# Kernel tuning notes

Measured on AMD Instinct MI355X. Metric: run time of the kernel, lower is better.

## Reference

```python
import jax, jax.numpy as jnp
import numpy as np

NUM_HEADS = 16
HEAD_DIM = 64
HIDDEN = NUM_HEADS * HEAD_DIM  # 1024
B, T = 32, 512


def setup_inputs() -> dict:
    key = jax.random.key(0)
    ks = jax.random.split(key, 10)
    s = 1.0 / np.sqrt(HIDDEN)
    inp = {
        "x": jax.random.normal(ks[0], (B, HIDDEN, T), dtype=jnp.float32),
        "mask": jax.random.randint(ks[1], (B, T), 0, 2, dtype=jnp.int32),
        "Wq": jax.random.uniform(ks[2], (HIDDEN, HIDDEN), jnp.float32, -s, s),
        "bq": jax.random.uniform(ks[3], (HIDDEN,), jnp.float32, -s, s),
        "Wk": jax.random.uniform(ks[4], (HIDDEN, HIDDEN), jnp.float32, -s, s),
        "bk": jax.random.uniform(ks[5], (HIDDEN,), jnp.float32, -s, s),
        "Wv": jax.random.uniform(ks[6], (HIDDEN, HIDDEN), jnp.float32, -s, s),
        "bv": jax.random.uniform(ks[7], (HIDDEN,), jnp.float32, -s, s),
        "Wo": jax.random.uniform(ks[8], (HIDDEN, HIDDEN), jnp.float32, -s, s),
        "bo": jax.random.uniform(ks[9], (HIDDEN,), jnp.float32, -s, s),
    }
    return inp


def reference(x, mask, Wq, bq, Wk, bk, Wv, bv, Wo, bo):
    # x: [B, hidden, T] -> tokens along last axis
    b, h, t = x.shape
    xt = jnp.swapaxes(x, 1, 2)  # [B, T, hidden]

    def heads(w, bias):
        y = xt @ w.T + bias                       # [B, T, hidden]
        return y.reshape(b, t, NUM_HEADS, HEAD_DIM).transpose(0, 2, 1, 3)  # [B, nh, T, hd]

    q = heads(Wq, bq)
    k = heads(Wk, bk)
    v = heads(Wv, bv)

    scores = jnp.einsum("bhqd,bhkd->bhqk", q, k) / jnp.sqrt(jnp.float32(HEAD_DIM))
    # masked_fill(mask==0, -inf) then clamp to [-50, 50]: masked entries become -50
    scores = jnp.where(mask[:, None, None, :] == 0, -jnp.inf, scores)
    scores = jnp.clip(scores, -50.0, 50.0)
    attn = jax.nn.softmax(scores, axis=-1)        # [B, nh, T, T]
    out = jnp.einsum("bhqk,bhkd->bhqd", attn, v)  # [B, nh, T, hd]
    out = out.transpose(0, 2, 1, 3).reshape(b, t, h)
    out = out @ Wo.T + bo                         # [B, T, hidden]
    return out.max(axis=1)                        # [B, hidden]
```

## Files before the change

kernel.cpp:

```cpp
#include <hip/hip_runtime.h>


typedef _Float16 half8 __attribute__((ext_vector_type(8)));
typedef _Float16 half4 __attribute__((ext_vector_type(4)));
typedef float floatx4 __attribute__((ext_vector_type(4)));
typedef unsigned uintx2 __attribute__((ext_vector_type(2)));

#define HID 1024
#define TT 512
#define NB 32
#define QSCALE 0.1803368801111244f
#define SB2 72.13475204444817f

__device__ __forceinline__ void gload16(const void* g, void* l) {
    __builtin_amdgcn_global_load_lds(
        (const __attribute__((address_space(1))) unsigned int*)g,
        (__attribute__((address_space(3))) unsigned int*)l, 16, 0, 0);
}

__device__ __forceinline__ unsigned fkey(float f) {
    unsigned u = __float_as_uint(f);
    return (u & 0x80000000u) ? ~u : (u | 0x80000000u);
}
__device__ __forceinline__ float funkey(unsigned k) {
    unsigned u = (k & 0x80000000u) ? (k ^ 0x80000000u) : ~k;
    return __uint_as_float(u);
}

__global__ __launch_bounds__(256) void prep_kernel(
    const float* __restrict__ Wq, const float* __restrict__ Wk,
    const float* __restrict__ Wv, const float* __restrict__ Wo,
    _Float16* __restrict__ Wcat,
    const float* __restrict__ x, _Float16* __restrict__ xT,
    unsigned* __restrict__ omax,
    const float* __restrict__ bq, float* __restrict__ bqs,
    const int* __restrict__ mask, short* __restrict__ cp16,
    int* __restrict__ Tcg, _Float16* __restrict__ KT,
    _Float16* __restrict__ Vb)
{
    __shared__ float tile[64][65];
    const int bid = blockIdx.x;
    if (bid < 4096) {
        int i4 = bid * 256 + threadIdx.x;
        int sec = i4 >> 18;
        int off4 = i4 & ((1 << 18) - 1);
        const float* src = (sec == 0) ? Wq : (sec == 1) ? Wk
                          : (sec == 2) ? Wv : Wo;
        float4 v = ((const float4*)src)[off4];
        if (sec == 0) {
            v.x *= QSCALE; v.y *= QSCALE; v.z *= QSCALE; v.w *= QSCALE;
        }
        half4 h = {(_Float16)v.x, (_Float16)v.y, (_Float16)v.z, (_Float16)v.w};
        *(half4*)(Wcat + (size_t)i4 * 4) = h;
    } else if (bid < 8192) {
        int idx = bid - 4096;
        int b = idx >> 7, h0 = ((idx >> 3) & 15) * 64, t0 = (idx & 7) * 64;
        int tx = threadIdx.x & 15, ty = threadIdx.x >> 4;
        const float* xb = x + ((size_t)b * HID + h0) * TT + t0;
        for (int p = 0; p < 4; p++) {
            int r = ty + 16 * p;
            float4 v = *(const float4*)(xb + (size_t)r * TT + tx * 4);
            tile[r][tx * 4 + 0] = v.x;
            tile[r][tx * 4 + 1] = v.y;
            tile[r][tx * 4 + 2] = v.z;
            tile[r][tx * 4 + 3] = v.w;
        }
        __syncthreads();
        int hc = (threadIdx.x & 7) * 8, tb = threadIdx.x >> 3;
        for (int rd = 0; rd < 2; rd++) {
            int tt = tb + 32 * rd;
            half8 pk;
            for (int k = 0; k < 8; k++)
                pk[k] = (_Float16)tile[hc + k][tt];
            *(half8*)(xT + ((size_t)b * TT + t0 + tt) * HID + h0 + hc) = pk;
        }
    } else if (bid < 8320) {
        omax[(bid - 8192) * 256 + threadIdx.x] = 0u;
    } else if (bid < 8324) {
        int i = (bid - 8320) * 256 + threadIdx.x;
        bqs[i] = bq[i] * QSCALE;
    } else {
        __shared__ int wsum[4];
        __shared__ int tcs;
        const int b = bid - 8324;
        const int* mrow = mask + b * TT;
        const int tid = threadIdx.x;
        const int lane = tid & 63, wv = tid >> 6;
        const int m0 = mrow[tid * 2] ? 1 : 0;
        const int m1 = mrow[tid * 2 + 1] ? 1 : 0;
        const int ps = m0 + m1;
        int v = ps;
        for (int d = 1; d < 64; d <<= 1) {
            int u = __shfl_up(v, d, 64);
            if (lane >= d) v += u;
        }
        if (lane == 63) wsum[wv] = v;
        __syncthreads();
        int off = 0;
        for (int i = 0; i < 4; i++) off += (i < wv) ? wsum[i] : 0;
        const int excl = off + v - ps;
        cp16[(size_t)b * TT + tid * 2]     = m0 ? (short)excl : (short)-1;
        cp16[(size_t)b * TT + tid * 2 + 1] = m1 ? (short)(excl + m0) : (short)-1;
        if (tid == 255) { tcs = off + v; Tcg[b] = off + v; }
        __syncthreads();
        const int Tcv = tcs;
        const int ce = (Tcv + 63) & ~63;
        const int nrow = ce - Tcv;
        half8 z8 = {};
        _Float16* kb = KT + ((size_t)b * TT + Tcv) * HID;
        for (int i = tid; i < nrow * 128; i += 256) ((half8*)kb)[i] = z8;
        for (int o = tid; o < 1024; o += 256) {
            _Float16* vr = Vb + ((size_t)b * HID + o) * TT;
            for (int j = 0; j < nrow; j++) vr[Tcv + j] = (_Float16)0.f;
        }
    }
}

#define PH_PRE do { \
    __builtin_amdgcn_s_barrier(); \
    asm volatile("s_waitcnt lgkmcnt(0)" ::: "memory"); \
    __builtin_amdgcn_sched_barrier(0); \
    __builtin_amdgcn_s_setprio(1); \
} while (0)

#define PH_POST(N) do { \
    __builtin_amdgcn_s_setprio(0); \
    asm volatile("s_waitcnt vmcnt(" #N ")" ::: "memory"); \
    __builtin_amdgcn_s_barrier(); \
} while (0)

#define LDA(P, MH) do { \
    const _Float16* ab_ = lds + (P) * 16384 + (MH) * 8192 + aoff; \
    af[0][0] = *(const half8*)(ab_ + pb0); \
    af[0][1] = *(const half8*)(ab_ + pb1); \
    af[1][0] = *(const half8*)(ab_ + 1024 + pb0); \
    af[1][1] = *(const half8*)(ab_ + 1024 + pb1); \
    af[2][0] = *(const half8*)(ab_ + 2048 + pb0); \
    af[2][1] = *(const half8*)(ab_ + 2048 + pb1); \
    af[3][0] = *(const half8*)(ab_ + 3072 + pb0); \
    af[3][1] = *(const half8*)(ab_ + 3072 + pb1); \
} while (0)

#define LDB(P, NH) do { \
    const _Float16* bb_ = lds + 32768 + (P) * 16384 + (NH) * 8192 + boff; \
    bf[NH][0][0] = *(const half8*)(bb_ + pb0); \
    bf[NH][0][1] = *(const half8*)(bb_ + pb1); \
    bf[NH][1][0] = *(const half8*)(bb_ + 1024 + pb0); \
    bf[NH][1][1] = *(const half8*)(bb_ + 1024 + pb1); \
} while (0)

#define MFMAQ(MH, NH) do { \
    _Pragma("unroll") \
    for (int j_ = 0; j_ < 4; ++j_) { \
        _Pragma("unroll") \
        for (int n_ = 0; n_ < 2; ++n_) { \
            floatx4 c_ = acc[(MH) * 4 + j_][(NH) * 2 + n_]; \
            c_ = __builtin_amdgcn_mfma_f32_16x16x32_f16( \
                af[j_][0], bf[NH][n_][0], c_, 0, 0, 0); \
            c_ = __builtin_amdgcn_mfma_f32_16x16x32_f16( \
                af[j_][1], bf[NH][n_][1], c_, 0, 0, 0); \
            acc[(MH) * 4 + j_][(NH) * 2 + n_] = c_; \
        } \
    } \
} while (0)

#define STAGE_A(P, MH, K0) do { \
    _Float16* d_ = lds + (P) * 16384 + (MH) * 8192 + wst; \
    gload16(ag + (MH) * 65536 + (K0), d_); \
    gload16(ag + 131072 + (MH) * 65536 + (K0), d_ + 4096); \
} while (0)

#define STAGE_B(P, NH, K0) do { \
    _Float16* d_ = lds + 32768 + (P) * 16384 + (NH) * 8192 + wst; \
    gload16(bg + (NH) * 32768 + (K0), d_); \
    gload16(bg + 131072 + (NH) * 32768 + (K0), d_ + 4096); \
} while (0)

__device__ __forceinline__ void mainloop256(
    const _Float16* __restrict__ Ag,
    const _Float16* __restrict__ Bg,
    _Float16* lds, floatx4 acc[8][4], int tid)
{
    const int lane = tid & 63;
    const int w = tid >> 6, wr = w >> 2, wc = w & 3;
    const int l15 = lane & 15, quad = lane >> 4;
    const int pa = quad ^ (l15 & 7);
    const int pb0 = pa * 8, pb1 = (pa ^ 4) * 8;
    const int aoff = (wr * 64 + l15) * 64;
    const int boff = (wc * 32 + l15) * 64;
    const int wst = w * 512;
    const int r = tid >> 3;
    const int sg = (tid & 7) ^ (r & 7);
    const int nbase = ((r >> 5) << 6) + (r & 31);
    const _Float16* ag = Ag + (size_t)r * 1024 + sg * 8;
    const _Float16* bg = Bg + (size_t)nbase * 1024 + sg * 8;

    half8 af[4][2], bf[2][2][2];

    STAGE_A(0, 0, 0); STAGE_B(0, 0, 0); STAGE_B(0, 1, 0); STAGE_A(0, 1, 0);
    STAGE_A(1, 0, 64); STAGE_B(1, 0, 64); STAGE_B(1, 1, 64);
    asm volatile("s_waitcnt vmcnt(10)" ::: "memory");
    __builtin_amdgcn_s_barrier();

    for (int i = 0; i < 7; ++i) {
        const int kb = i * 128 + 64;
        const int kn0 = kb + 64, kn1 = kb + 128;
        LDA(0, 0); LDB(0, 0); STAGE_A(1, 1, kb);
        PH_PRE; MFMAQ(0, 0); PH_POST(10);
        LDB(0, 1);            STAGE_A(0, 0, kn0);
        PH_PRE; MFMAQ(0, 1); PH_POST(10);
        LDA(0, 1);            STAGE_B(0, 0, kn0);
        PH_PRE; MFMAQ(1, 1); PH_POST(10);
                              STAGE_B(0, 1, kn0);
        PH_PRE; MFMAQ(1, 0); PH_POST(10);
        LDA(1, 0); LDB(1, 0); STAGE_A(0, 1, kn0);
        PH_PRE; MFMAQ(0, 0); PH_POST(10);
        LDB(1, 1);            STAGE_A(1, 0, kn1);
        PH_PRE; MFMAQ(0, 1); PH_POST(10);
        LDA(1, 1);            STAGE_B(1, 0, kn1);
        PH_PRE; MFMAQ(1, 1); PH_POST(10);
                              STAGE_B(1, 1, kn1);
        PH_PRE; MFMAQ(1, 0); PH_POST(10);
    }
    LDA(0, 0); LDB(0, 0); STAGE_A(1, 1, 960);
    PH_PRE; MFMAQ(0, 0); PH_POST(10);
    LDB(0, 1);
    PH_PRE; MFMAQ(0, 1); PH_POST(8);
    LDA(0, 1);
    PH_PRE; MFMAQ(1, 1); PH_POST(6);
    PH_PRE; MFMAQ(1, 0); PH_POST(4);
    LDA(1, 0); LDB(1, 0);
    PH_PRE; MFMAQ(0, 0); PH_POST(2);
    LDB(1, 1);
    PH_PRE; MFMAQ(0, 1); PH_POST(0);
    LDA(1, 1);
    PH_PRE; MFMAQ(1, 1); MFMAQ(1, 0);
    __builtin_amdgcn_s_setprio(0);
}

__global__ __launch_bounds__(512, 2) void gemm1_kernel(
    const _Float16* __restrict__ Wcat,
    const float* __restrict__ bqs, const float* __restrict__ bk,
    const float* __restrict__ bv,
    const _Float16* __restrict__ xT,
    _Float16* __restrict__ QT, _Float16* __restrict__ KT,
    _Float16* __restrict__ Vb, const short* __restrict__ cp16)
{
    __shared__ __align__(16) _Float16 smem[65536];
    const int tid = threadIdx.x;
    const int id = blockIdx.x;
    const int xcd = id & 7, slot = id >> 3;
    const int grp = xcd + 8 * (slot / 12);
    const int m0 = (slot % 12) * 256;
    const int n0 = (grp & 1) * 256;
    const int bb = grp >> 1;
    const int lane = tid & 63;
    const int w = tid >> 6, wr = w >> 2, wc = w & 3;
    const int l15 = lane & 15, quad = lane >> 4;

    floatx4 acc[8][4] = {};
    mainloop256(Wcat + (size_t)m0 * 1024,
                xT + ((size_t)bb * TT + n0) * HID, smem, acc, tid);
    __syncthreads();

    const int sec = m0 >> 10;
    const int mo = m0 & 1023;

    if (sec < 2) {
        const float* bias = (sec == 0) ? bqs : bk;
        _Float16* dst = (sec == 0) ? QT : KT;
        _Float16* tr = smem;
        for (int h = 0; h < 2; ++h) {
            if (wr == h) {
                for (int mi = 0; mi < 8; ++mi) {
                    float bs[4];
                    for (int rr = 0; rr < 4; ++rr)
                        bs[rr] = bias[mo + h * 128 + mi * 16 + quad * 4 + rr];
                    for (int ni = 0; ni < 4; ++ni) {
                        half4 pk;
                        for (int rr = 0; rr < 4; ++rr)
                            pk[rr] = (_Float16)(acc[mi][ni][rr] + bs[rr]);
                        *(half4*)(tr + (wc * 64 + ni * 16 + l15) * 136 +
                                  mi * 16 + quad * 4) = pk;
                    }
                }
            }
            __syncthreads();
            const int row = tid >> 4, off = (tid & 15) * 8;
            for (int s = 0; s < 8; ++s) {
                uint4 v = *(uint4*)(tr + (row + 32 * s) * 136 + off);
                if (sec == 0) {
                    *(uint4*)(dst + ((size_t)bb * TT + n0 + row + 32 * s) * HID +
                              mo + h * 128 + off) = v;
                } else {
                    short cp = cp16[bb * TT + n0 + row + 32 * s];
                    if (cp >= 0)
                        *(uint4*)(dst + ((size_t)bb * TT + cp) * HID +
                                  mo + h * 128 + off) = v;
                }
            }
            __syncthreads();
        }
    } else {
        short cps[4];
        for (int ni = 0; ni < 4; ++ni)
            cps[ni] = cp16[bb * TT + n0 + wc * 64 + ni * 16 + l15];
        for (int mi = 0; mi < 8; ++mi) {
            float bs[4];
            for (int rr = 0; rr < 4; ++rr)
                bs[rr] = bv[mo + wr * 128 + mi * 16 + quad * 4 + rr];
            for (int ni = 0; ni < 4; ++ni) {
                if (cps[ni] < 0) continue;
                for (int rr = 0; rr < 4; ++rr) {
                    int o = mo + wr * 128 + mi * 16 + quad * 4 + rr;
                    Vb[((size_t)bb * HID + o) * TT + cps[ni]] =
                        (_Float16)(acc[mi][ni][rr] + bs[rr]);
                }
            }
        }
    }
}

__global__ __launch_bounds__(512, 4) void attn_kernel(
    const _Float16* __restrict__ QT, const _Float16* __restrict__ KT,
    const _Float16* __restrict__ Vb, const int* __restrict__ Tcg,
    _Float16* __restrict__ OcT)
{
    __shared__ __align__(16) _Float16 kvbuf[4 * 4096];
    __shared__ __align__(16) _Float16 ps[2 * 8192];
    __shared__ __align__(16) float msf[2][64];

    const int id = blockIdx.x;
    const int xcd = id & 7, slot = id >> 3;
    const int grp = xcd + 8 * (slot >> 1);
    const int q0 = (slot & 1) * 256;
    const int hd = grp & 15, b = grp >> 4;
    const int tid = threadIdx.x;
    const int lane = tid & 63, wid = tid >> 6;
    const int l15 = lane & 15, quad = lane >> 4;

    const _Float16* QTb = QT + ((size_t)b * TT + q0) * HID + hd * 64;
    const _Float16* KTb = KT + (size_t)b * TT * HID + hd * 64;
    const _Float16* Vbb = Vb + ((size_t)b * HID + hd * 64) * TT;
    const int Tc = Tcg[b];
    const int nt = (Tc + 63) >> 6;

    const int srow = lane >> 3;
    const int sg = (lane & 7) ^ srow;
    const int pa = quad ^ (l15 & 7);
    const int pz = l15 & 7;

    for (int p = 0; p < 4; p++) {
        int r = p * 64 + wid * 8 + srow;
        gload16(QTb + (size_t)r * HID + sg * 8,
                kvbuf + (p * 64 + wid * 8) * 64);
    }
    __syncthreads();
    half8 bq[2][2];
    for (int qt = 0; qt < 2; qt++) {
        int qr = qt * 128 + wid * 16 + l15;
        bq[qt][0] = *(half8*)(kvbuf + qr * 64 + pa * 8);
        bq[qt][1] = *(half8*)(kvbuf + qr * 64 + (pa ^ 4) * 8);
    }
    __syncthreads();

    auto stage = [&](int jcn, int bufn) {
        int t0n = jcn * 64;
        _Float16* kd = kvbuf + bufn * 4096;
        _Float16* vd = kvbuf + (2 + bufn) * 4096;
        int r = wid * 8 + srow;
        gload16(KTb + (size_t)(t0n + r) * HID + sg * 8, kd + (wid * 8) * 64);
        gload16(Vbb + (size_t)r * TT + t0n + sg * 8, vd + (wid * 8) * 64);
        if (tid < 64) msf[bufn][tid] = (t0n + tid < Tc) ? SB2 : -SB2;
    };

    stage(0, 0);

    floatx4 oacc[2][4] = {};
    float rs[2] = {0.f, 0.f};
    const float lo = -SB2;

    for (int jc = 0; jc < nt; jc++) {
        const int cur = jc & 1;
        __syncthreads();
        if (jc < nt - 1) stage(jc + 1, 1 - cur);

        const _Float16* ks = kvbuf + cur * 4096;
        const _Float16* vs = kvbuf + (2 + cur) * 4096;

        for (int jt = 0; jt < 4; jt++) {
            half8 ka0 = *(half8*)(ks + (jt * 16 + l15) * 64 + pa * 8);
            half8 ka1 = *(half8*)(ks + (jt * 16 + l15) * 64 + (pa ^ 4) * 8);
            floatx4 hi = *(floatx4*)(&msf[cur][jt * 16 + quad * 4]);
            for (int qt = 0; qt < 2; qt++) {
                floatx4 sc = {0.f, 0.f, 0.f, 0.f};
                sc = __builtin_amdgcn_mfma_f32_16x16x32_f16(ka0, bq[qt][0], sc, 0, 0, 0);
                sc = __builtin_amdgcn_mfma_f32_16x16x32_f16(ka1, bq[qt][1], sc, 0, 0, 0);
                float e0 = __builtin_amdgcn_exp2f(fminf(fmaxf(sc[0], lo), hi[0]));
                float e1 = __builtin_amdgcn_exp2f(fminf(fmaxf(sc[1], lo), hi[1]));
                float e2 = __builtin_amdgcn_exp2f(fminf(fmaxf(sc[2], lo), hi[2]));
                float e3 = __builtin_amdgcn_exp2f(fminf(fmaxf(sc[3], lo), hi[3]));
                rs[qt] += (e0 + e1) + (e2 + e3);
                unsigned uA = __builtin_bit_cast(
                    unsigned, __builtin_amdgcn_cvt_pkrtz(e0, e1));
                unsigned uB = __builtin_bit_cast(
                    unsigned, __builtin_amdgcn_cvt_pkrtz(e2, e3));
                uintx2 uv = {uA, uB};
                half4 pk = __builtin_bit_cast(half4, uv);
                int g = jt * 2 + (quad >> 1);
                *(half4*)(ps + qt * 8192 + (wid * 16 + l15) * 64 + (g ^ pz) * 8 +
                          (quad & 1) * 4) = pk;
            }
        }
        for (int kc = 0; kc < 2; kc++) {
            int g = kc * 4 + quad;
            half8 bv8[4];
            for (int d4 = 0; d4 < 4; d4++)
                bv8[d4] = *(half8*)(vs + (d4 * 16 + l15) * 64 + (g ^ pz) * 8);
            for (int qt = 0; qt < 2; qt++) {
                half8 ap = *(half8*)(ps + qt * 8192 + (wid * 16 + l15) * 64 +
                                     (g ^ pz) * 8);
                for (int d4 = 0; d4 < 4; d4++)
                    oacc[qt][d4] = __builtin_amdgcn_mfma_f32_16x16x32_f16(
                        ap, bv8[d4], oacc[qt][d4], 0, 0, 0);
            }
        }
    }

    for (int qt = 0; qt < 2; qt++) {
        float s = rs[qt];
        s += __shfl_xor(s, 16, 64);
        s += __shfl_xor(s, 32, 64);
        s = 1.0f / s;
        float inv[4];
        for (int r = 0; r < 4; r++) inv[r] = __shfl(s, quad * 4 + r, 64);
        for (int d4 = 0; d4 < 4; d4++)
            for (int r = 0; r < 4; r++) {
                int t = q0 + qt * 128 + wid * 16 + quad * 4 + r;
                int c = hd * 64 + d4 * 16 + l15;
                OcT[((size_t)b * TT + t) * HID + c] =
                    (_Float16)(oacc[qt][d4][r] * inv[r]);
            }
    }
}

__global__ __launch_bounds__(512, 2) void gemm2_kernel(
    const _Float16* __restrict__ Wo16, const _Float16* __restrict__ OcT,
    unsigned* __restrict__ omax)
{
    __shared__ __align__(16) _Float16 smem[65536];
    _Float16* lds = smem;
    const int tid = threadIdx.x;
    const int id = blockIdx.x;
    const int xcd = id & 7, slot = id >> 3;
    const int grp = xcd + 8 * (slot >> 2);
    const int m0 = (slot & 3) * 256;
    const int n0 = (grp & 1) * 256;
    const int bb = grp >> 1;
    const int lane = tid & 63;
    const int w = tid >> 6, wr = w >> 2;
    const int l15 = lane & 15, quad = lane >> 4;

    floatx4 acc[8][4] = {};
    mainloop256(Wo16 + (size_t)m0 * 1024,
                OcT + ((size_t)bb * TT + n0) * HID, lds, acc, tid);

    for (int mi = 0; mi < 8; ++mi)
        for (int rr = 0; rr < 4; ++rr) {
            float v = acc[mi][0][rr];
            v = fmaxf(v, acc[mi][1][rr]);
            v = fmaxf(v, acc[mi][2][rr]);
            v = fmaxf(v, acc[mi][3][rr]);
            for (int d = 1; d < 16; d <<= 1)
                v = fmaxf(v, __shfl_xor(v, d, 64));
            if (l15 == 0) {
                int o = m0 + wr * 128 + mi * 16 + quad * 4 + rr;
                atomicMax(&omax[bb * HID + o], fkey(v));
            }
        }
}

__global__ __launch_bounds__(256) void final_kernel(
    const unsigned* __restrict__ omax, const float* __restrict__ bo,
    float* __restrict__ out)
{
    int i = blockIdx.x * 256 + threadIdx.x;
    out[i] = funkey(omax[i]) + bo[i & 1023];
}

extern "C" void kernel_launch(void* const* d_in, const int* in_sizes, int n_in,
                              void* d_out, int out_size, void* d_ws, size_t ws_size,
                              hipStream_t stream)
{
    const float* x  = (const float*)d_in[0];
    const int* mask = (const int*)d_in[1];
    const float* Wq = (const float*)d_in[2];
    const float* bq = (const float*)d_in[3];
    const float* Wk = (const float*)d_in[4];
    const float* bk = (const float*)d_in[5];
    const float* Wv = (const float*)d_in[6];
    const float* bv = (const float*)d_in[7];
    const float* Wo = (const float*)d_in[8];
    const float* bo = (const float*)d_in[9];
    float* out = (float*)d_out;

    char* ws = (char*)d_ws;
    _Float16* Wcat = (_Float16*)(ws);
    _Float16* xT   = (_Float16*)(ws + (8ull  << 20));
    _Float16* QT   = (_Float16*)(ws + (40ull << 20));
    _Float16* KT   = (_Float16*)(ws + (72ull << 20));
    _Float16* Vb   = (_Float16*)(ws + (104ull << 20));
    _Float16* OcT  = (_Float16*)(ws + (136ull << 20));
    unsigned* omax = (unsigned*)(ws + (168ull << 20));
    float*    bqs  = (float*)(ws + (168ull << 20) + (128ull << 10));
    short*    cp16 = (short*)(ws + (168ull << 20) + (132ull << 10));
    int*      Tcg  = (int*)  (ws + (168ull << 20) + (164ull << 10));

    prep_kernel<<<8356, 256, 0, stream>>>(Wq, Wk, Wv, Wo, Wcat, x, xT, omax,
                                          bq, bqs, mask, cp16, Tcg, KT, Vb);
    gemm1_kernel<<<768, 512, 0, stream>>>(Wcat, bqs, bk, bv, xT, QT, KT, Vb,
                                          cp16);
    attn_kernel<<<1024, 512, 0, stream>>>(QT, KT, Vb, Tcg, OcT);
    gemm2_kernel<<<256, 512, 0, stream>>>(Wcat + (3ull << 20), OcT, omax);
    final_kernel<<<128, 256, 0, stream>>>(omax, bo, out);
}
```

Baseline: 320.2 us.

## Compact unmasked tokens before K/V projection and skip empty GEMM tiles

The mask prefix scan moves into its own small kernel that runs first, so the prep kernel can scatter the unmasked tokens of x into a compacted buffer (reusing the OcT workspace). The K and V projection tiles then read this compacted input and return early for column blocks past the padded valid-token count, which avoids the matrix work on masked keys. This adds an extra kernel launch and a serial dependency ahead of prep, plus extra scattered writes of xTc.

```diff
diff --git a/kernel.cpp b/kernel.cpp
--- a/kernel.cpp
+++ b/kernel.cpp
@@ -27,16 +27,55 @@
     return __uint_as_float(u);
 }
 
+__global__ __launch_bounds__(256) void scan_kernel(
+    const int* __restrict__ mask, short* __restrict__ cp16,
+    int* __restrict__ Tcg, _Float16* __restrict__ KT,
+    _Float16* __restrict__ Vb)
+{
+    __shared__ int wsum[4];
+    __shared__ int tcs;
+    const int b = blockIdx.x;
+    const int* mrow = mask + b * TT;
+    const int tid = threadIdx.x;
+    const int lane = tid & 63, wv = tid >> 6;
+    const int m0 = mrow[tid * 2] ? 1 : 0;
+    const int m1 = mrow[tid * 2 + 1] ? 1 : 0;
+    const int ps = m0 + m1;
+    int v = ps;
+    for (int d = 1; d < 64; d <<= 1) {
+        int u = __shfl_up(v, d, 64);
+        if (lane >= d) v += u;
+    }
+    if (lane == 63) wsum[wv] = v;
+    __syncthreads();
+    int off = 0;
+    for (int i = 0; i < 4; i++) off += (i < wv) ? wsum[i] : 0;
+    const int excl = off + v - ps;
+    cp16[(size_t)b * TT + tid * 2]     = m0 ? (short)excl : (short)-1;
+    cp16[(size_t)b * TT + tid * 2 + 1] = m1 ? (short)(excl + m0) : (short)-1;
+    if (tid == 255) { tcs = off + v; Tcg[b] = off + v; }
+    __syncthreads();
+    const int Tcv = tcs;
+    const int ce = (Tcv + 63) & ~63;
+    const int nrow = ce - Tcv;
+    half8 z8 = {};
+    _Float16* kb = KT + ((size_t)b * TT + Tcv) * HID;
+    for (int i = tid; i < nrow * 128; i += 256) ((half8*)kb)[i] = z8;
+    for (int o = tid; o < 1024; o += 256) {
+        _Float16* vr = Vb + ((size_t)b * HID + o) * TT;
+        for (int j = 0; j < nrow; j++) vr[Tcv + j] = (_Float16)0.f;
+    }
+}
+
 __global__ __launch_bounds__(256) void prep_kernel(
     const float* __restrict__ Wq, const float* __restrict__ Wk,
     const float* __restrict__ Wv, const float* __restrict__ Wo,
     _Float16* __restrict__ Wcat,
     const float* __restrict__ x, _Float16* __restrict__ xT,
+    _Float16* __restrict__ xTc,
     unsigned* __restrict__ omax,
     const float* __restrict__ bq, float* __restrict__ bqs,
-    const int* __restrict__ mask, short* __restrict__ cp16,
-    int* __restrict__ Tcg, _Float16* __restrict__ KT,
-    _Float16* __restrict__ Vb)
+    const short* __restrict__ cp16)
 {
     __shared__ float tile[64][65];
     const int bid = blockIdx.x;
@@ -73,46 +112,15 @@
             for (int k = 0; k < 8; k++)
                 pk[k] = (_Float16)tile[hc + k][tt];
             *(half8*)(xT + ((size_t)b * TT + t0 + tt) * HID + h0 + hc) = pk;
+            short ct = cp16[b * TT + t0 + tt];
+            if (ct >= 0)
+                *(half8*)(xTc + ((size_t)b * TT + ct) * HID + h0 + hc) = pk;
         }
     } else if (bid < 8320) {
         omax[(bid - 8192) * 256 + threadIdx.x] = 0u;
-    } else if (bid < 8324) {
+    } else {
         int i = (bid - 8320) * 256 + threadIdx.x;
         bqs[i] = bq[i] * QSCALE;
-    } else {
-        __shared__ int wsum[4];
-        __shared__ int tcs;
-        const int b = bid - 8324;
-        const int* mrow = mask + b * TT;
-        const int tid = threadIdx.x;
-        const int lane = tid & 63, wv = tid >> 6;
-        const int m0 = mrow[tid * 2] ? 1 : 0;
-        const int m1 = mrow[tid * 2 + 1] ? 1 : 0;
-        const int ps = m0 + m1;
-        int v = ps;
-        for (int d = 1; d < 64; d <<= 1) {
-            int u = __shfl_up(v, d, 64);
-            if (lane >= d) v += u;
-        }
-        if (lane == 63) wsum[wv] = v;
-        __syncthreads();
-        int off = 0;
-        for (int i = 0; i < 4; i++) off += (i < wv) ? wsum[i] : 0;
-        const int excl = off + v - ps;
-        cp16[(size_t)b * TT + tid * 2]     = m0 ? (short)excl : (short)-1;
-        cp16[(size_t)b * TT + tid * 2 + 1] = m1 ? (short)(excl + m0) : (short)-1;
-        if (tid == 255) { tcs = off + v; Tcg[b] = off + v; }
-        __syncthreads();
-        const int Tcv = tcs;
-        const int ce = (Tcv + 63) & ~63;
-        const int nrow = ce - Tcv;
-        half8 z8 = {};
-        _Float16* kb = KT + ((size_t)b * TT + Tcv) * HID;
-        for (int i = tid; i < nrow * 128; i += 256) ((half8*)kb)[i] = z8;
-        for (int o = tid; o < 1024; o += 256) {
-            _Float16* vr = Vb + ((size_t)b * HID + o) * TT;
-            for (int j = 0; j < nrow; j++) vr[Tcv + j] = (_Float16)0.f;
-        }
     }
 }
 
@@ -242,9 +250,9 @@
     const _Float16* __restrict__ Wcat,
     const float* __restrict__ bqs, const float* __restrict__ bk,
     const float* __restrict__ bv,
-    const _Float16* __restrict__ xT,
+    const _Float16* __restrict__ xT, const _Float16* __restrict__ xTc,
     _Float16* __restrict__ QT, _Float16* __restrict__ KT,
-    _Float16* __restrict__ Vb, const short* __restrict__ cp16)
+    _Float16* __restrict__ Vb, const int* __restrict__ Tcg)
 {
     __shared__ __align__(16) _Float16 smem[65536];
     const int tid = threadIdx.x;
@@ -258,12 +266,16 @@
     const int w = tid >> 6, wr = w >> 2, wc = w & 3;
     const int l15 = lane & 15, quad = lane >> 4;
 
+    const int sec = m0 >> 10;
+    const int Tc = Tcg[bb];
+    if (sec > 0 && n0 >= ((Tc + 255) & ~255)) return;
+
     floatx4 acc[8][4] = {};
     mainloop256(Wcat + (size_t)m0 * 1024,
-                xT + ((size_t)bb * TT + n0) * HID, smem, acc, tid);
+                ((sec == 0) ? xT : xTc) + ((size_t)bb * TT + n0) * HID,
+                smem, acc, tid);
     __syncthreads();
 
-    const int sec = m0 >> 10;
     const int mo = m0 & 1023;
 
     if (sec < 2) {
@@ -288,32 +300,25 @@
             __syncthreads();
             const int row = tid >> 4, off = (tid & 15) * 8;
             for (int s = 0; s < 8; ++s) {
+                int trow = n0 + row + 32 * s;
                 uint4 v = *(uint4*)(tr + (row + 32 * s) * 136 + off);
-                if (sec == 0) {
-                    *(uint4*)(dst + ((size_t)bb * TT + n0 + row + 32 * s) * HID +
+                if (sec == 0 || trow < Tc)
+                    *(uint4*)(dst + ((size_t)bb * TT + trow) * HID +
                               mo + h * 128 + off) = v;
-                } else {
-                    short cp = cp16[bb * TT + n0 + row + 32 * s];
-                    if (cp >= 0)
-                        *(uint4*)(dst + ((size_t)bb * TT + cp) * HID +
-                                  mo + h * 128 + off) = v;
-                }
             }
             __syncthreads();
         }
     } else {
-        short cps[4];
-        for (int ni = 0; ni < 4; ++ni)
-            cps[ni] = cp16[bb * TT + n0 + wc * 64 + ni * 16 + l15];
         for (int mi = 0; mi < 8; ++mi) {
             float bs[4];
             for (int rr = 0; rr < 4; ++rr)
                 bs[rr] = bv[mo + wr * 128 + mi * 16 + quad * 4 + rr];
             for (int ni = 0; ni < 4; ++ni) {
-                if (cps[ni] < 0) continue;
+                int t = n0 + wc * 64 + ni * 16 + l15;
+                if (t >= Tc) continue;
                 for (int rr = 0; rr < 4; ++rr) {
                     int o = mo + wr * 128 + mi * 16 + quad * 4 + rr;
-                    Vb[((size_t)bb * HID + o) * TT + cps[ni]] =
+                    Vb[((size_t)bb * HID + o) * TT + t] =
                         (_Float16)(acc[mi][ni][rr] + bs[rr]);
                 }
             }
@@ -511,15 +516,17 @@
     _Float16* KT   = (_Float16*)(ws + (72ull << 20));
     _Float16* Vb   = (_Float16*)(ws + (104ull << 20));
     _Float16* OcT  = (_Float16*)(ws + (136ull << 20));
+    _Float16* xTc  = OcT;
     unsigned* omax = (unsigned*)(ws + (168ull << 20));
     float*    bqs  = (float*)(ws + (168ull << 20) + (128ull << 10));
     short*    cp16 = (short*)(ws + (168ull << 20) + (132ull << 10));
     int*      Tcg  = (int*)  (ws + (168ull << 20) + (164ull << 10));
 
-    prep_kernel<<<8356, 256, 0, stream>>>(Wq, Wk, Wv, Wo, Wcat, x, xT, omax,
-                                          bq, bqs, mask, cp16, Tcg, KT, Vb);
-    gemm1_kernel<<<768, 512, 0, stream>>>(Wcat, bqs, bk, bv, xT, QT, KT, Vb,
-                                          cp16);
+    scan_kernel<<<32, 256, 0, stream>>>(mask, cp16, Tcg, KT, Vb);
+    prep_kernel<<<8324, 256, 0, stream>>>(Wq, Wk, Wv, Wo, Wcat, x, xT, xTc,
+                                          omax, bq, bqs, cp16);
+    gemm1_kernel<<<768, 512, 0, stream>>>(Wcat, bqs, bk, bv, xT, xTc,
+                                          QT, KT, Vb, Tcg);
     attn_kernel<<<1024, 512, 0, stream>>>(QT, KT, Vb, Tcg, OcT);
     gemm2_kernel<<<256, 512, 0, stream>>>(Wcat + (3ull << 20), OcT, omax);
     final_kernel<<<128, 256, 0, stream>>>(omax, bo, out);
```

Result: no change. 320.7 us (+0.1%).
